# Performance work log

Measured on AMD Instinct MI355X. Metric: run time of the kernel, lower is better.

The kernel has to match this reference:

```python
import jax, jax.numpy as jnp
import numpy as np

EPS = 1e-3       # module eps for mask normalization
LN_EPS = 1e-5    # torch LayerNorm default eps


def _layernorm(x, w, b):
    mu = jnp.mean(x, axis=-1, keepdims=True)
    var = jnp.var(x, axis=-1, keepdims=True)
    return (x - mu) * jax.lax.rsqrt(var + LN_EPS) * w + b


def setup_inputs() -> dict:
    key = jax.random.key(0)
    ks = jax.random.split(key, 8)
    N_seq, N_res, c_m, c_h, c_z = 256, 256, 256, 32, 128
    m = jax.random.normal(ks[0], (N_seq, N_res, c_m), jnp.float32)
    mask = jnp.ones((N_seq, N_res), jnp.float32)
    s_m = 1.0 / np.sqrt(c_m)
    ln_w = jnp.ones((c_m,), jnp.float32)
    ln_b = jnp.zeros((c_m,), jnp.float32)
    w1 = jax.random.normal(ks[1], (c_m, c_h), jnp.float32) * s_m
    b1 = jnp.zeros((c_h,), jnp.float32)
    w2 = jax.random.normal(ks[2], (c_m, c_h), jnp.float32) * s_m
    b2 = jnp.zeros((c_h,), jnp.float32)
    # linear_out has init='final' (zeros) in training; use small random so the
    # reference output / gradients are non-trivial for kernel testing.
    w_out = jax.random.normal(ks[3], (c_h * c_h, c_z), jnp.float32) * 0.02
    b_out = jnp.zeros((c_z,), jnp.float32)
    return {"m": m, "mask": mask, "ln_w": ln_w, "ln_b": ln_b,
            "w1": w1, "b1": b1, "w2": w2, "b2": b2,
            "w_out": w_out, "b_out": b_out}


def reference(m, mask, ln_w, ln_b, w1, b1, w2, b2, w_out, b_out):
    # m: [N_seq, N_res, c_m], mask: [N_seq, N_res]
    ln = _layernorm(m, ln_w, ln_b)
    mk = mask[..., None]                                 # [S, N, 1]
    a = (ln @ w1 + b1) * mk                              # [S, N, h]
    b = (ln @ w2 + b2) * mk                              # [S, N, h]
    a = jnp.swapaxes(a, -2, -3)                          # [N, S, h]
    b = jnp.swapaxes(b, -2, -3)                          # [N, S, h]
    # outer product mean over sequences: [N, N, h, h]
    outer = jnp.einsum('isc,jse->ijce', a, b)
    N = outer.shape[0]
    outer = outer.reshape(N, N, -1)                      # [N, N, h*h]
    out = outer @ w_out + b_out                          # [N, N, c_z]
    norm = jnp.einsum('si,sj->ij', mask, mask) + EPS     # [N, N]
    return out / norm[..., None]
```

## Files before the change

kernel.cpp:

```cpp
#include <hip/hip_runtime.h>
#include <hip/hip_bf16.h>
#include <stdint.h>

typedef __bf16 bf16x8 __attribute__((ext_vector_type(8)));
typedef float  f32x4  __attribute__((ext_vector_type(4)));
typedef float  f32x16 __attribute__((ext_vector_type(16)));
typedef __attribute__((address_space(1))) uint32_t u32_g;
typedef __attribute__((address_space(3))) uint32_t u32_l;
typedef unsigned short u16;
typedef u16 u16x4 __attribute__((ext_vector_type(4)));

__device__ __forceinline__ void gload16(const void* g, void* l) {
    __builtin_amdgcn_global_load_lds((u32_g*)g, (u32_l*)l, 16, 0, 0);
}

__device__ __forceinline__ u16 bf16bits(float v) {
    __bf16 h = (__bf16)v;
    return __builtin_bit_cast(u16, h);
}

#define WAITV(n) asm volatile("s_waitcnt vmcnt(" #n ")" ::: "memory")
#define BAR() do { __builtin_amdgcn_s_barrier(); \
                   __builtin_amdgcn_sched_barrier(0); } while (0)

__global__ __launch_bounds__(256) void k_prep(const float* __restrict__ w_out,
                                              const float* __restrict__ mask,
                                              const float* __restrict__ w1,
                                              const float* __restrict__ w2,
                                              u16* __restrict__ WT,
                                              u16* __restrict__ WcatT,
                                              float* __restrict__ rnormv) {
    __shared__ float mcol[256];
    const int b = blockIdx.x, t = threadIdx.x;
    if (b < 512) {
        int idx = b * 256 + t;
        int z = idx >> 10, kc = idx & 1023;
        int c = kc & 31, e = kc >> 5;
        WT[idx] = bf16bits(w_out[(c * 32 + e) * 128 + z]);
    } else if (b < 576) {
        int idx = (b - 512) * 256 + t;
        int n = idx >> 8, k = idx & 255;
        float v = (n < 32) ? w1[k * 32 + n] : w2[k * 32 + (n - 32)];
        WcatT[idx] = bf16bits(v);
    } else {
        int i = b - 576;
        mcol[t] = mask[(size_t)t * 256 + i];
        __syncthreads();
        float acc = 1e-3f;
#pragma unroll 8
        for (int s = 0; s < 256; ++s)
            acc += mcol[s] * mask[(size_t)s * 256 + t];
        rnormv[i * 256 + t] = 1.0f / acc;
    }
}

__global__ __launch_bounds__(256, 2) void k_lnproj(
        const float* __restrict__ M, const float* __restrict__ mask,
        const float* __restrict__ lnw, const float* __restrict__ lnb,
        const float* __restrict__ b1, const float* __restrict__ b2,
        const u16* __restrict__ WcatT,
        u16* __restrict__ AT, u16* __restrict__ BT) {
    __shared__ __align__(16) u16 sh[32768];
    const int tid = threadIdx.x, lane = tid & 63, w = tid >> 6;
    const int i = blockIdx.x, s0 = blockIdx.y * 64;

#pragma unroll
    for (int p = 0; p < 8; ++p) {
        int flat = p * 256 + tid;
        int r = flat >> 5, slot = flat & 31;
        int gs = slot ^ (r & 7);
        const char* src = (const char*)WcatT + (size_t)r * 512 + (size_t)gs * 16;
        char* dst = (char*)sh + 32768 + (size_t)(p * 256 + (tid & ~63)) * 16;
        gload16(src, dst);
    }

    float4 wv = *(const float4*)(lnw + lane * 4);
    float4 bv = *(const float4*)(lnb + lane * 4);
    float4 xv[16];
#pragma unroll
    for (int it = 0; it < 16; ++it) {
        int s = s0 + w * 16 + it;
        xv[it] = *(const float4*)(M + ((size_t)s * 256 + i) * 256 + lane * 4);
    }
#pragma unroll
    for (int it = 0; it < 16; ++it) {
        int row = w * 16 + it;
        float4 x = xv[it];
        float s1 = x.x + x.y + x.z + x.w;
        float s2 = x.x * x.x + x.y * x.y + x.z * x.z + x.w * x.w;
#pragma unroll
        for (int o = 1; o < 64; o <<= 1) {
            s1 += __shfl_xor(s1, o);
            s2 += __shfl_xor(s2, o);
        }
        float mu   = s1 * 0.00390625f;
        float var  = s2 * 0.00390625f - mu * mu;
        float rstd = rsqrtf(var + 1e-5f);
        u16x4 pk;
        pk[0] = bf16bits((x.x - mu) * rstd * wv.x + bv.x);
        pk[1] = bf16bits((x.y - mu) * rstd * wv.y + bv.y);
        pk[2] = bf16bits((x.z - mu) * rstd * wv.z + bv.z);
        pk[3] = bf16bits((x.w - mu) * rstd * wv.w + bv.w);
        int byte = (row * 512 + lane * 8) ^ ((row & 7) << 4);
        *(u16x4*)((char*)sh + byte) = pk;
    }
    __syncthreads();

    f32x4 acc[4] = {};
#pragma unroll
    for (int kk = 0; kk < 8; ++kk) {
        int kb = kk * 64 + ((lane >> 4) << 4);
        int arow = w * 16 + (lane & 15);
        bf16x8 af = *(const bf16x8*)((const char*)sh +
                     ((arow * 512 + kb) ^ ((arow & 7) << 4)));
#pragma unroll
        for (int f = 0; f < 4; ++f) {
            int nrow = f * 16 + (lane & 15);
            bf16x8 bfr = *(const bf16x8*)((const char*)sh + 32768 +
                          ((nrow * 512 + kb) ^ ((nrow & 7) << 4)));
            acc[f] = __builtin_amdgcn_mfma_f32_16x16x32_bf16(af, bfr, acc[f], 0, 0, 0);
        }
    }

    const int sb = s0 + w * 16 + ((lane >> 4) << 2);
    float mk[4];
#pragma unroll
    for (int r = 0; r < 4; ++r) mk[r] = mask[(size_t)(sb + r) * 256 + i];
#pragma unroll
    for (int f = 0; f < 4; ++f) {
        int col = f * 16 + (lane & 15);
        float bias = (col < 32) ? b1[col] : b2[col - 32];
        u16* dst = ((col < 32) ? AT : BT) + ((size_t)i * 32 + (col & 31)) * 256 + sb;
        u16x4 pk;
#pragma unroll
        for (int r = 0; r < 4; ++r)
            pk[r] = bf16bits((acc[f][r] + bias) * mk[r]);
        *(u16x4*)dst = pk;
    }
}

__global__ __launch_bounds__(512, 4) void k_fused(
        const u16* __restrict__ AT, const u16* __restrict__ BT,
        const u16* __restrict__ WT, const float* __restrict__ rnormv,
        const float* __restrict__ b_out, float* __restrict__ out) {
    __shared__ __align__(16) u16 sh[36864];
    const int tid  = threadIdx.x;
    const int lane = tid & 63;
    const int wid  = tid >> 6;
    const int wr   = wid >> 2, wc = wid & 3;
    const int l15  = lane & 15;
    const int q16  = lane >> 4;
    const int lid = blockIdx.x;
    const int swz = (lid & 7) * 256 + (lid >> 3);
    const int bx = swz & 63, by = swz >> 6;
    const int m0 = bx * 128, n0 = by * 256;

    f32x4 acc[4][4] = {};

    auto stage = [&](int kt, int buf) {
        char* base = (char*)sh + buf * 24576;
        const int k0 = kt * 32;
        {
            int r = tid >> 2, slot = tid & 3;
            int gs = slot ^ ((r >> 1) & 3);
            gload16((const char*)AT + (((size_t)(m0 + r)) * 256 + k0) * 2 + gs * 16,
                    base + (size_t)(tid & ~63) * 16);
        }
#pragma unroll
        for (int q = 0; q < 2; ++q) {
            int flat = q * 512 + tid;
            int r = flat >> 2, slot = flat & 3;
            int gs = slot ^ ((r >> 1) & 3);
            gload16((const char*)BT + (((size_t)(n0 + r)) * 256 + k0) * 2 + gs * 16,
                    base + 8192 + (size_t)(q * 512 + (tid & ~63)) * 16);
        }
    };

    auto compute = [&](int buf) {
        const char* Ab = (const char*)sh + buf * 24576;
        const char* Bb = Ab + 8192;
        bf16x8 af[4], bfr[4];
#pragma unroll
        for (int mi = 0; mi < 4; ++mi) {
            int rA = wr * 64 + mi * 16 + l15;
            af[mi] = *(const bf16x8*)(Ab + rA * 64 + (q16 ^ ((rA >> 1) & 3)) * 16);
        }
#pragma unroll
        for (int nj = 0; nj < 4; ++nj) {
            int rB = wc * 64 + nj * 16 + l15;
            bfr[nj] = *(const bf16x8*)(Bb + rB * 64 + (q16 ^ ((rB >> 1) & 3)) * 16);
        }
        __builtin_amdgcn_s_setprio(1);
#pragma unroll
        for (int mi = 0; mi < 4; ++mi)
#pragma unroll
            for (int nj = 0; nj < 4; ++nj)
                acc[mi][nj] = __builtin_amdgcn_mfma_f32_16x16x32_bf16(
                    af[mi], bfr[nj], acc[mi][nj], 0, 0, 0);
        __builtin_amdgcn_s_setprio(0);
    };

    stage(0, 0);
    stage(1, 1);
    WAITV(3);
    BAR();
#pragma unroll
    for (int t = 0; t < 8; ++t) {
        if (t + 2 < 8) stage(t + 2, (t + 2) % 3);
        compute(t % 3);
        if (t < 6) { WAITV(3); }
        else if (t == 6) { WAITV(0); }
        BAR();
    }

#pragma unroll
    for (int mi = 0; mi < 4; ++mi)
#pragma unroll
        for (int nj = 0; nj < 4; ++nj) {
            int m = wr * 64 + mi * 16 + (q16 << 2);
            int n = wc * 64 + nj * 16 + l15;
            int pr = ((m >> 5) << 3) | (n >> 5);
            int c0 = m & 31, e = n & 31;
            int byte = pr * 2048 + (e * 32 + c0) * 2;
            byte ^= ((pr ^ e) & 7) << 4;
            u16x4 pk;
#pragma unroll
            for (int r = 0; r < 4; ++r)
                pk[r] = bf16bits(acc[mi][nj][r]);
            *(u16x4*)((char*)sh + byte) = pk;
        }
    __syncthreads();

    if (wid < 4) {
        const int z0  = wid * 32;
        const int hi  = lane >> 5;
        const int p32 = lane & 31;
        const u16* wtrow = WT + (size_t)(z0 + p32) * 1024 + hi * 8;

        f32x16 a0 = {}, a1 = {};
        bf16x8 wbr[8];
#pragma unroll
        for (int d = 0; d < 8; ++d)
            wbr[d] = *(const bf16x8*)(wtrow + d * 16);

        auto paddr = [&](int ks) {
            int kc = ks * 16 + hi * 8;
            int byte = p32 * 2048 + kc * 2;
            byte ^= ((p32 ^ (kc >> 5)) & 7) << 4;
            return (const bf16x8*)((const char*)sh + byte);
        };
        bf16x8 pa0 = *paddr(0), pa1 = *paddr(1);

#pragma unroll
        for (int ks = 0; ks < 64; ++ks) {
            bf16x8 cur = (ks & 1) ? pa1 : pa0;
            if (ks + 2 < 64) {
                if (ks & 1) pa1 = *paddr(ks + 2);
                else        pa0 = *paddr(ks + 2);
            }
            if (ks & 1)
                a1 = __builtin_amdgcn_mfma_f32_32x32x16_bf16(cur, wbr[ks & 7], a1, 0, 0, 0);
            else
                a0 = __builtin_amdgcn_mfma_f32_32x32x16_bf16(cur, wbr[ks & 7], a0, 0, 0, 0);
            if (ks + 8 < 64)
                wbr[ks & 7] = *(const bf16x8*)(wtrow + (ks + 8) * 16);
        }

        const int i0 = bx * 4, j0 = by * 8;
        const int z  = z0 + p32;
        const float bz = b_out[z];
#pragma unroll
        for (int r = 0; r < 16; ++r) {
            int pair = (r & 3) + 8 * (r >> 2) + 4 * hi;
            int i = i0 + (pair >> 3), j = j0 + (pair & 7);
            float val = (a0[r] + a1[r] + bz) * rnormv[i * 256 + j];
            out[((size_t)(i * 256 + j)) * 128 + z] = val;
        }
    }
}

extern "C" void kernel_launch(void* const* d_in, const int* in_sizes, int n_in,
                              void* d_out, int out_size, void* d_ws, size_t ws_size,
                              hipStream_t stream) {
    const float* M    = (const float*)d_in[0];
    const float* mask = (const float*)d_in[1];
    const float* lnw  = (const float*)d_in[2];
    const float* lnb  = (const float*)d_in[3];
    const float* w1   = (const float*)d_in[4];
    const float* b1   = (const float*)d_in[5];
    const float* w2   = (const float*)d_in[6];
    const float* b2   = (const float*)d_in[7];
    const float* wout = (const float*)d_in[8];
    const float* bout = (const float*)d_in[9];
    float* out = (float*)d_out;

    char* ws = (char*)d_ws;
    u16*   AT    = (u16*)(ws);
    u16*   BT    = (u16*)(ws + 4194304);
    u16*   WT    = (u16*)(ws + 8388608);
    float* rnormv= (float*)(ws + 8650752);
    u16*   WcatT = (u16*)(ws + 8912896);

    k_prep  <<<832, 256, 0, stream>>>(wout, mask, w1, w2, WT, WcatT, rnormv);
    k_lnproj<<<dim3(256, 4), 256, 0, stream>>>(M, mask, lnw, lnb, b1, b2, WcatT, AT, BT);
    k_fused <<<2048, 512, 0, stream>>>(AT, BT, WT, rnormv, bout, out);
}
```

Baseline: 118.3 us.

## Split epilogue GEMM across all eight waves with LDS reduction; retile block mapping

```diff
diff --git a/kernel.cpp b/kernel.cpp
--- a/kernel.cpp
+++ b/kernel.cpp
@@ -151,8 +151,10 @@
     const int l15  = lane & 15;
     const int q16  = lane >> 4;
     const int lid = blockIdx.x;
-    const int swz = (lid & 7) * 256 + (lid >> 3);
-    const int bx = swz & 63, by = swz >> 6;
+    const int x   = lid & 7;
+    const int kk_ = lid >> 3;
+    const int bx  = (x & 3) * 16 + (kk_ & 15);
+    const int by  = (x >> 2) * 16 + (kk_ >> 4);
     const int m0 = bx * 128, n0 = by * 256;
 
     f32x4 acc[4][4] = {};
@@ -231,50 +233,64 @@
         }
     __syncthreads();
 
-    if (wid < 4) {
-        const int z0  = wid * 32;
-        const int hi  = lane >> 5;
-        const int p32 = lane & 31;
-        const u16* wtrow = WT + (size_t)(z0 + p32) * 1024 + hi * 8;
-
-        f32x16 a0 = {}, a1 = {};
-        bf16x8 wbr[8];
-#pragma unroll
-        for (int d = 0; d < 8; ++d)
-            wbr[d] = *(const bf16x8*)(wtrow + d * 16);
-
-        auto paddr = [&](int ks) {
-            int kc = ks * 16 + hi * 8;
-            int byte = p32 * 2048 + kc * 2;
-            byte ^= ((p32 ^ (kc >> 5)) & 7) << 4;
-            return (const bf16x8*)((const char*)sh + byte);
-        };
-        bf16x8 pa0 = *paddr(0), pa1 = *paddr(1);
-
-#pragma unroll
-        for (int ks = 0; ks < 64; ++ks) {
-            bf16x8 cur = (ks & 1) ? pa1 : pa0;
-            if (ks + 2 < 64) {
-                if (ks & 1) pa1 = *paddr(ks + 2);
-                else        pa0 = *paddr(ks + 2);
-            }
-            if (ks & 1)
-                a1 = __builtin_amdgcn_mfma_f32_32x32x16_bf16(cur, wbr[ks & 7], a1, 0, 0, 0);
-            else
-                a0 = __builtin_amdgcn_mfma_f32_32x32x16_bf16(cur, wbr[ks & 7], a0, 0, 0, 0);
-            if (ks + 8 < 64)
-                wbr[ks & 7] = *(const bf16x8*)(wtrow + (ks + 8) * 16);
-        }
-
+    const int slice = wid & 3;
+    const int half  = wid >> 2;
+    const int z0  = slice * 32;
+    const int hi  = lane >> 5;
+    const int p32 = lane & 31;
+    const u16* wtrow = WT + (size_t)(z0 + p32) * 1024 + half * 512 + hi * 8;
+
+    f32x16 a0 = {}, a1 = {};
+    bf16x8 wbr[8];
+#pragma unroll
+    for (int d = 0; d < 8; ++d)
+        wbr[d] = *(const bf16x8*)(wtrow + d * 16);
+
+    auto paddr = [&](int ks) {
+        int kc = half * 512 + ks * 16 + hi * 8;
+        int byte = p32 * 2048 + kc * 2;
+        byte ^= ((p32 ^ (kc >> 5)) & 7) << 4;
+        return (const bf16x8*)((const char*)sh + byte);
+    };
+    bf16x8 pa0 = *paddr(0), pa1 = *paddr(1);
+
+#pragma unroll
+    for (int ks = 0; ks < 32; ++ks) {
+        bf16x8 cur = (ks & 1) ? pa1 : pa0;
+        if (ks + 2 < 32) {
+            if (ks & 1) pa1 = *paddr(ks + 2);
+            else        pa0 = *paddr(ks + 2);
+        }
+        if (ks & 1)
+            a1 = __builtin_amdgcn_mfma_f32_32x32x16_bf16(cur, wbr[ks & 7], a1, 0, 0, 0);
+        else
+            a0 = __builtin_amdgcn_mfma_f32_32x32x16_bf16(cur, wbr[ks & 7], a0, 0, 0, 0);
+        if (ks + 8 < 32)
+            wbr[ks & 7] = *(const bf16x8*)(wtrow + (ks + 8) * 16);
+    }
+#pragma unroll
+    for (int r = 0; r < 16; ++r) a0[r] += a1[r];
+
+    __syncthreads();
+    float* red = (float*)sh;
+    if (half == 1) {
+#pragma unroll
+        for (int r = 0; r < 16; ++r)
+            red[slice * 1024 + r * 64 + lane] = a0[r];
+    }
+    __syncthreads();
+
+    if (half == 0) {
         const int i0 = bx * 4, j0 = by * 8;
         const int z  = z0 + p32;
         const float bz = b_out[z];
 #pragma unroll
         for (int r = 0; r < 16; ++r) {
+            float v = a0[r] + red[slice * 1024 + r * 64 + lane];
             int pair = (r & 3) + 8 * (r >> 2) + 4 * hi;
             int i = i0 + (pair >> 3), j = j0 + (pair & 7);
-            float val = (a0[r] + a1[r] + bz) * rnormv[i * 256 + j];
-            out[((size_t)(i * 256 + j)) * 128 + z] = val;
+            out[((size_t)(i * 256 + j)) * 128 + z] =
+                (v + bz) * rnormv[i * 256 + j];
         }
     }
 }
```

After: 118.2 us. No clear change (-0.0%).
